# Optimization experiments

Measured on AMD Instinct MI355X. Metric: run time of the kernel, lower is better.

Reference implementation:

```python
import jax, jax.numpy as jnp
import numpy as np

N_NODES = 200_000
N_EDGES = 6_400_000
N_GRAPHS = 512


def _sage_conv(x, edge_index, Wl, bl, Wr):
    """PyG SAGEConv (mean aggr): lin_l(mean_j x_j) + lin_r(x_i).
    lin_l has bias, lin_r does not. Messages flow src -> dst."""
    src, dst = edge_index[0], edge_index[1]
    n = x.shape[0]
    # gather neighbor features [E, F] and segment-mean into dst nodes
    msg_sum = jax.ops.segment_sum(x[src], dst, num_segments=n)
    deg = jax.ops.segment_sum(jnp.ones((src.shape[0],), x.dtype), dst, num_segments=n)
    mean = msg_sum / jnp.maximum(deg, 1.0)[:, None]  # zero in-degree -> 0
    return mean @ Wl.T + bl + x @ Wr.T


def setup_inputs() -> dict:
    key = jax.random.key(0)
    ks = jax.random.split(key, 9)
    x = jax.random.normal(ks[0], (N_NODES, 1), dtype=jnp.float32)
    edge_index = jax.random.randint(ks[1], (2, N_EDGES), 0, N_NODES, dtype=jnp.int64)
    batch = jnp.sort(jax.random.randint(ks[2], (N_NODES,), 0, N_GRAPHS, dtype=jnp.int64))
    W1l = jax.random.normal(ks[3], (16, 1), dtype=jnp.float32)
    b1 = jax.random.normal(ks[4], (16,), dtype=jnp.float32)
    W1r = jax.random.normal(ks[5], (16, 1), dtype=jnp.float32)
    W2l = jax.random.normal(ks[6], (1, 16), dtype=jnp.float32)
    b2 = jax.random.normal(ks[7], (1,), dtype=jnp.float32)
    W2r = jax.random.normal(ks[8], (1, 16), dtype=jnp.float32)
    return {"x": x, "edge_index": edge_index, "batch": batch, "batch_size": N_GRAPHS,
            "W1l": W1l, "b1": b1, "W1r": W1r, "W2l": W2l, "b2": b2, "W2r": W2r}


def reference(x, edge_index, batch, batch_size, W1l, b1, W1r, W2l, b2, W2r):
    h = _sage_conv(x, edge_index, W1l, b1, W1r)          # [N, 16]
    h = jax.nn.relu(h)
    h = _sage_conv(h, edge_index, W2l, b2, W2r)          # [N, 1]
    # global_add_pool: segment-sum node features by graph id
    out = jax.ops.segment_sum(h, batch, num_segments=batch_size)  # [B, 1]
    return out
```

## Files before the change

kernel.cpp:

```cpp
#include <hip/hip_runtime.h>


#define PP        16
#define BLK       1024
#define SCAP      1024u
#define SMASK     1023u
#define TILE      (BLK * 4)
#define CBIN      16
#define CNT_ONE   (1u << 25)
#define FX_BIAS   131072
#define SCALE     4096.0f
#define INV_SCALE (1.0f / 4096.0f)

__global__ __launch_bounds__(BLK) void partition_kernel(
    const int* __restrict__ ei, const float* __restrict__ x,
    unsigned* __restrict__ xq1, unsigned* __restrict__ pairs,
    unsigned* __restrict__ tails, int E, int N, int bins, unsigned Mdiv,
    int cap) {
    extern __shared__ unsigned buf[];
    __shared__ unsigned cnt[PP], base[PP], fq[PP], gb[PP];
    const int tid = threadIdx.x;
    if (tid < PP) { cnt[tid] = 0; base[tid] = 0; }

    for (int n = blockIdx.x * BLK + tid; n < N; n += gridDim.x * BLK)
        xq1[n] = CNT_ONE + (unsigned)((int)rintf(x[n] * SCALE) + FX_BIAS);
    __syncthreads();

    int b0 = blockIdx.x * TILE;
    int e0 = b0 + tid * 4;
    int nv = E - e0; nv = nv < 0 ? 0 : (nv > 4 ? 4 : nv);
    int srcv[4], dstv[4];
    if (nv == 4 && ((E & 3) == 0)) {
        int4 s = *(const int4*)(ei + e0);
        int4 d = *(const int4*)(ei + E + e0);
        srcv[0] = s.x; srcv[1] = s.y; srcv[2] = s.z; srcv[3] = s.w;
        dstv[0] = d.x; dstv[1] = d.y; dstv[2] = d.z; dstv[3] = d.w;
    } else {
        for (int j = 0; j < nv; ++j) { srcv[j] = ei[e0 + j]; dstv[j] = ei[E + e0 + j]; }
    }
    unsigned w[4]; int part[4]; bool pend[4];
    for (int j = 0; j < 4; ++j) {
        pend[j] = (j < nv);
        if (pend[j]) {
            unsigned dst = (unsigned)dstv[j];
            unsigned pt = (unsigned)(((unsigned long long)dst * Mdiv) >> 32);
            int ld = (int)dst - (int)pt * bins;
            while (ld >= bins) { ld -= bins; ++pt; }
            while (ld < 0)     { ld += bins; --pt; }
            part[j] = (int)pt;
            w[j] = ((unsigned)srcv[j] << 14) | (unsigned)ld;
        }
    }
    for (int j = 0; j < 4; ++j) {
        if (pend[j]) {
            unsigned slot = atomicAdd(&cnt[part[j]], 1u);
            if (slot - base[part[j]] < SCAP) {
                buf[part[j] * SCAP + (slot & SMASK)] = w[j]; pend[j] = false;
            } else atomicSub(&cnt[part[j]], 1u);
        }
    }
    int npend = __syncthreads_count((int)(pend[0] | pend[1] | pend[2] | pend[3]));
    while (npend > 0) {
        if (tid < PP) {
            unsigned avail = cnt[tid] - base[tid];
            unsigned f = avail & ~511u;
            fq[tid] = f;
            if (f) gb[tid] = atomicAdd(&tails[tid], f);
        }
        __syncthreads();
        {
            int wv = tid >> 6, lane = tid & 63;
            unsigned f = fq[wv];
            if (f) {
                unsigned g0 = gb[wv], bs = base[wv];
                unsigned mx = (g0 + f <= (unsigned)cap) ? f : ((unsigned)cap > g0 ? (unsigned)cap - g0 : 0u);
                unsigned* dp = pairs + (size_t)wv * cap + g0;
                for (unsigned jj = lane; jj < mx; jj += 64)
                    dp[jj] = buf[wv * SCAP + ((bs + jj) & SMASK)];
            }
        }
        __syncthreads();
        if (tid < PP) base[tid] += fq[tid];
        __syncthreads();
        for (int j = 0; j < 4; ++j) {
            if (pend[j]) {
                unsigned slot = atomicAdd(&cnt[part[j]], 1u);
                if (slot - base[part[j]] < SCAP) {
                    buf[part[j] * SCAP + (slot & SMASK)] = w[j]; pend[j] = false;
                } else atomicSub(&cnt[part[j]], 1u);
            }
        }
        npend = __syncthreads_count((int)(pend[0] | pend[1] | pend[2] | pend[3]));
    }
    if (tid < PP) {
        unsigned avail = cnt[tid] - base[tid];
        fq[tid] = avail;
        if (avail) gb[tid] = atomicAdd(&tails[tid], avail);
    }
    __syncthreads();
    {
        int wv = tid >> 6, lane = tid & 63;
        unsigned f = fq[wv];
        if (f) {
            unsigned g0 = gb[wv], bs = base[wv];
            unsigned mx = (g0 + f <= (unsigned)cap) ? f : ((unsigned)cap > g0 ? (unsigned)cap - g0 : 0u);
            unsigned* dp = pairs + (size_t)wv * cap + g0;
            for (unsigned jj = lane; jj < mx; jj += 64)
                dp[jj] = buf[wv * SCAP + ((bs + jj) & SMASK)];
        }
    }
}

__global__ __launch_bounds__(BLK) void bin1_kernel(
    const unsigned* __restrict__ pairs, const unsigned* __restrict__ tails,
    const unsigned* __restrict__ xq1, unsigned* __restrict__ slab,
    int N, int bins, int cap) {
    extern __shared__ unsigned sb[];
    int p = blockIdx.x & (PP - 1);
    int c = blockIdx.x / PP;
    int len = (int)tails[p]; if (len > cap) len = cap;
    int st = (int)((long long)len * c / CBIN);
    int en = (int)((long long)len * (c + 1) / CBIN);
    for (int j = threadIdx.x; j < bins; j += BLK) sb[j] = 0;
    __syncthreads();
    const unsigned* bp = pairs + (size_t)p * cap;
    int st4 = (st + 3) & ~3;
    int en4 = en & ~3;
    int preEnd = st4 < en ? st4 : en;
    for (int e = st + (int)threadIdx.x; e < preEnd; e += BLK) {
        unsigned wv = bp[e];
        atomicAdd(&sb[wv & 16383u], xq1[wv >> 14]);
    }
    if (st4 < en4) {
        const uint4* bp4 = (const uint4*)(bp + st4);
        int n4 = (en4 - st4) >> 2;
        for (int e = threadIdx.x; e < n4; e += BLK) {
            uint4 wq = bp4[e];
            unsigned p0 = xq1[wq.x >> 14];
            unsigned p1 = xq1[wq.y >> 14];
            unsigned p2 = xq1[wq.z >> 14];
            unsigned p3 = xq1[wq.w >> 14];
            atomicAdd(&sb[wq.x & 16383u], p0);
            atomicAdd(&sb[wq.y & 16383u], p1);
            atomicAdd(&sb[wq.z & 16383u], p2);
            atomicAdd(&sb[wq.w & 16383u], p3);
        }
    }
    int tailSt = st4 > en4 ? st4 : en4;
    for (int e = tailSt + (int)threadIdx.x; e < en; e += BLK) {
        unsigned wv = bp[e];
        atomicAdd(&sb[wv & 16383u], xq1[wv >> 14]);
    }
    __syncthreads();
    unsigned* dst = slab + (size_t)c * N + (size_t)p * bins;
    int nb = N - p * bins; if (nb > bins) nb = bins;
    for (int j = threadIdx.x; j < nb; j += BLK) dst[j] = sb[j];
}

__global__ __launch_bounds__(BLK) void bin2_kernel(
    const unsigned* __restrict__ pairs, const unsigned* __restrict__ tails,
    const int* __restrict__ pvq, int* __restrict__ slab,
    int N, int bins, int cap) {
    extern __shared__ int sbi[];
    int p = blockIdx.x & (PP - 1);
    int c = blockIdx.x / PP;
    int len = (int)tails[p]; if (len > cap) len = cap;
    int st = (int)((long long)len * c / CBIN);
    int en = (int)((long long)len * (c + 1) / CBIN);
    for (int j = threadIdx.x; j < bins; j += BLK) sbi[j] = 0;
    __syncthreads();
    const unsigned* bp = pairs + (size_t)p * cap;
    int st4 = (st + 3) & ~3;
    int en4 = en & ~3;
    int preEnd = st4 < en ? st4 : en;
    for (int e = st + (int)threadIdx.x; e < preEnd; e += BLK) {
        unsigned wv = bp[e];
        atomicAdd(&sbi[wv & 16383u], pvq[wv >> 14]);
    }
    if (st4 < en4) {
        const uint4* bp4 = (const uint4*)(bp + st4);
        int n4 = (en4 - st4) >> 2;
        for (int e = threadIdx.x; e < n4; e += BLK) {
            uint4 wq = bp4[e];
            int p0 = pvq[wq.x >> 14];
            int p1 = pvq[wq.y >> 14];
            int p2 = pvq[wq.z >> 14];
            int p3 = pvq[wq.w >> 14];
            atomicAdd(&sbi[wq.x & 16383u], p0);
            atomicAdd(&sbi[wq.y & 16383u], p1);
            atomicAdd(&sbi[wq.z & 16383u], p2);
            atomicAdd(&sbi[wq.w & 16383u], p3);
        }
    }
    int tailSt = st4 > en4 ? st4 : en4;
    for (int e = tailSt + (int)threadIdx.x; e < en; e += BLK) {
        unsigned wv = bp[e];
        atomicAdd(&sbi[wv & 16383u], pvq[wv >> 14]);
    }
    __syncthreads();
    int* dst = slab + (size_t)c * N + (size_t)p * bins;
    int nb = N - p * bins; if (nb > bins) nb = bins;
    for (int j = threadIdx.x; j < nb; j += BLK) dst[j] = sbi[j];
}

__global__ void node_pass1_kernel(const float* __restrict__ x,
                                  const unsigned* __restrict__ slab,
                                  const float* __restrict__ W1l,
                                  const float* __restrict__ b1,
                                  const float* __restrict__ W1r,
                                  const float* __restrict__ W2l,
                                  const float* __restrict__ W2r,
                                  float* __restrict__ deg_out,
                                  int* __restrict__ pvq,
                                  float* __restrict__ qv,
                                  int N) {
    __shared__ float s_w1l[16], s_b1[16], s_w1r[16], s_w2l[16], s_w2r[16];
    if (threadIdx.x < 16) {
        s_w1l[threadIdx.x] = W1l[threadIdx.x];
        s_b1[threadIdx.x]  = b1[threadIdx.x];
        s_w1r[threadIdx.x] = W1r[threadIdx.x];
        s_w2l[threadIdx.x] = W2l[threadIdx.x];
        s_w2r[threadIdx.x] = W2r[threadIdx.x];
    }
    __syncthreads();
    int n = blockIdx.x * blockDim.x + threadIdx.x;
    if (n >= N) return;

    unsigned cnt = 0, fx = 0;
#pragma unroll
    for (int c = 0; c < CBIN; ++c) {
        unsigned w = slab[(size_t)c * N + n];
        cnt += w >> 25;
        fx  += w & (CNT_ONE - 1);
    }
    float dg  = (float)cnt;
    float sum = (float)(int)(fx - cnt * (unsigned)FX_BIAS) * INV_SCALE;
    float m   = sum / fmaxf(dg, 1.0f);

    float xv = x[n];
    float pa = 0.0f, qa = 0.0f;
#pragma unroll
    for (int f = 0; f < 16; ++f) {
        float h = fmaf(m, s_w1l[f], fmaf(xv, s_w1r[f], s_b1[f]));
        h = fmaxf(h, 0.0f);
        pa = fmaf(h, s_w2l[f], pa);
        qa = fmaf(h, s_w2r[f], qa);
    }
    deg_out[n] = dg;
    pvq[n] = (int)rintf(pa * SCALE);
    qv[n] = qa;
}

__global__ void node_pass2_kernel(const int* __restrict__ slab2,
                                  const float* __restrict__ deg,
                                  const float* __restrict__ qv,
                                  const float* __restrict__ b2,
                                  const int* __restrict__ batch,
                                  float* __restrict__ out,
                                  int N) {
    int i = blockIdx.x * blockDim.x + threadIdx.x;
    float b2v = b2[0];
    float val = 0.0f;
    int g;
    if (i < N) {
        int sacc = 0;
#pragma unroll
        for (int c = 0; c < CBIN; ++c) sacc += slab2[(size_t)c * N + i];
        float s2 = (float)sacc * INV_SCALE;
        val = s2 / fmaxf(deg[i], 1.0f) + b2v + qv[i];
        g = batch[i];
    } else {
        g = batch[N - 1];
    }
    int g0 = __shfl(g, 0);
    unsigned long long same = __ballot(g == g0);
    if (same == ~0ULL) {
        for (int off = 32; off > 0; off >>= 1) val += __shfl_down(val, off);
        if ((threadIdx.x & 63) == 0) atomicAdd(&out[g0], val);
    } else {
        atomicAdd(&out[g], val);
    }
}

extern "C" void kernel_launch(void* const* d_in, const int* in_sizes, int n_in,
                              void* d_out, int out_size, void* d_ws, size_t ws_size,
                              hipStream_t stream) {
    const float* x     = (const float*)d_in[0];
    const int*   ei    = (const int*)d_in[1];
    const int*   batch = (const int*)d_in[2];
    const float* W1l = (const float*)d_in[4];
    const float* b1  = (const float*)d_in[5];
    const float* W1r = (const float*)d_in[6];
    const float* W2l = (const float*)d_in[7];
    const float* b2  = (const float*)d_in[8];
    const float* W2r = (const float*)d_in[9];

    const int N = in_sizes[0];
    const int E = in_sizes[1] / 2;
    float* out = (float*)d_out;

    const int bins = (N + PP - 1) / PP;
    const unsigned Mdiv =
        (unsigned)(((1ULL << 32) + (unsigned)bins - 1) / (unsigned)bins);
    const int EperP = E / PP;
    int cap = ((EperP + EperP / 32 + 4096) + 1023) & ~1023;

    unsigned* pairs = (unsigned*)d_ws;
    unsigned* slab1 = pairs + (size_t)PP * cap;
    int*      slab2 = (int*)slab1;
    float* deg = (float*)(slab1 + (size_t)CBIN * N);
    int*   pvq = (int*)(deg + N);
    float* qv  = (float*)(pvq + N);
    unsigned* tails = (unsigned*)(qv + N);
    unsigned* xq1   = tails + PP;

    hipMemsetAsync(d_out, 0, (size_t)out_size * sizeof(float), stream);
    hipMemsetAsync(tails, 0, PP * sizeof(unsigned), stream);

    const int partShmem = PP * (int)SCAP * 4;
    const int binShmem  = bins * 4;
    hipFuncSetAttribute((const void*)partition_kernel,
                        hipFuncAttributeMaxDynamicSharedMemorySize, partShmem);
    hipFuncSetAttribute((const void*)bin1_kernel,
                        hipFuncAttributeMaxDynamicSharedMemorySize, binShmem);
    hipFuncSetAttribute((const void*)bin2_kernel,
                        hipFuncAttributeMaxDynamicSharedMemorySize, binShmem);

    int partBlocks = (E + TILE - 1) / TILE;
    const int NB = 256;
    int node_blocks = (N + NB - 1) / NB;

    partition_kernel<<<partBlocks, BLK, partShmem, stream>>>(ei, x, xq1, pairs,
                                                             tails, E, N, bins,
                                                             Mdiv, cap);
    bin1_kernel<<<PP * CBIN, BLK, binShmem, stream>>>(pairs, tails, xq1, slab1,
                                                      N, bins, cap);
    node_pass1_kernel<<<node_blocks, NB, 0, stream>>>(x, slab1, W1l, b1, W1r,
                                                      W2l, W2r, deg, pvq, qv, N);
    bin2_kernel<<<PP * CBIN, BLK, binShmem, stream>>>(pairs, tails, pvq, slab2,
                                                      N, bins, cap);
    node_pass2_kernel<<<node_blocks, NB, 0, stream>>>(slab2, deg, qv, b2, batch,
                                                      out, N);
}
```

Baseline: 219.8 us.

## Partition edges into 2D dst-by-src cells so bin kernels gather from LDS

Edges are now partitioned into 500 cells, split by destination partition (20) and by source block of 8192 nodes (25). Each bin block stages its source slice of features in shared memory, so the random gather of xq1/pvq reads LDS instead of global memory. The partition kernel becomes persistent with 512 blocks and uses a 32-entry ring per cell, which means more frequent flushes and a larger per-cell loop. In exchange, node passes sum 25 slabs instead of 16, cell capacity depends on a uniform-distribution estimate, and each cell flushes in small chunks.

```diff
diff --git a/kernel.cpp b/kernel.cpp
--- a/kernel.cpp
+++ b/kernel.cpp
@@ -1,12 +1,14 @@
 #include <hip/hip_runtime.h>
 
 
-#define PP        16
 #define BLK       1024
-#define SCAP      1024u
-#define SMASK     1023u
 #define TILE      (BLK * 4)
-#define CBIN      16
+#define NSB       25
+#define SBSH      13
+#define WMSK      8191u
+#define RING      32u
+#define RMSK      31u
+#define MAXC      512
 #define CNT_ONE   (1u << 25)
 #define FX_BIAS   131072
 #define SCALE     4096.0f
@@ -16,191 +18,180 @@
     const int* __restrict__ ei, const float* __restrict__ x,
     unsigned* __restrict__ xq1, unsigned* __restrict__ pairs,
     unsigned* __restrict__ tails, int E, int N, int bins, unsigned Mdiv,
-    int cap) {
+    int capC, int nc) {
     extern __shared__ unsigned buf[];
-    __shared__ unsigned cnt[PP], base[PP], fq[PP], gb[PP];
+    __shared__ unsigned cnt[MAXC], base[MAXC], fq[MAXC], gb[MAXC];
     const int tid = threadIdx.x;
-    if (tid < PP) { cnt[tid] = 0; base[tid] = 0; }
+    for (int j = tid; j < nc; j += BLK) { cnt[j] = 0; base[j] = 0; }
 
     for (int n = blockIdx.x * BLK + tid; n < N; n += gridDim.x * BLK)
         xq1[n] = CNT_ONE + (unsigned)((int)rintf(x[n] * SCALE) + FX_BIAS);
     __syncthreads();
 
-    int b0 = blockIdx.x * TILE;
-    int e0 = b0 + tid * 4;
-    int nv = E - e0; nv = nv < 0 ? 0 : (nv > 4 ? 4 : nv);
-    int srcv[4], dstv[4];
-    if (nv == 4 && ((E & 3) == 0)) {
-        int4 s = *(const int4*)(ei + e0);
-        int4 d = *(const int4*)(ei + E + e0);
-        srcv[0] = s.x; srcv[1] = s.y; srcv[2] = s.z; srcv[3] = s.w;
-        dstv[0] = d.x; dstv[1] = d.y; dstv[2] = d.z; dstv[3] = d.w;
-    } else {
-        for (int j = 0; j < nv; ++j) { srcv[j] = ei[e0 + j]; dstv[j] = ei[E + e0 + j]; }
-    }
-    unsigned w[4]; int part[4]; bool pend[4];
-    for (int j = 0; j < 4; ++j) {
-        pend[j] = (j < nv);
-        if (pend[j]) {
-            unsigned dst = (unsigned)dstv[j];
-            unsigned pt = (unsigned)(((unsigned long long)dst * Mdiv) >> 32);
-            int ld = (int)dst - (int)pt * bins;
-            while (ld >= bins) { ld -= bins; ++pt; }
-            while (ld < 0)     { ld += bins; --pt; }
-            part[j] = (int)pt;
-            w[j] = ((unsigned)srcv[j] << 14) | (unsigned)ld;
-        }
-    }
-    for (int j = 0; j < 4; ++j) {
-        if (pend[j]) {
-            unsigned slot = atomicAdd(&cnt[part[j]], 1u);
-            if (slot - base[part[j]] < SCAP) {
-                buf[part[j] * SCAP + (slot & SMASK)] = w[j]; pend[j] = false;
-            } else atomicSub(&cnt[part[j]], 1u);
-        }
-    }
-    int npend = __syncthreads_count((int)(pend[0] | pend[1] | pend[2] | pend[3]));
-    while (npend > 0) {
-        if (tid < PP) {
-            unsigned avail = cnt[tid] - base[tid];
-            unsigned f = avail & ~511u;
-            fq[tid] = f;
-            if (f) gb[tid] = atomicAdd(&tails[tid], f);
-        }
-        __syncthreads();
-        {
-            int wv = tid >> 6, lane = tid & 63;
-            unsigned f = fq[wv];
-            if (f) {
-                unsigned g0 = gb[wv], bs = base[wv];
-                unsigned mx = (g0 + f <= (unsigned)cap) ? f : ((unsigned)cap > g0 ? (unsigned)cap - g0 : 0u);
-                unsigned* dp = pairs + (size_t)wv * cap + g0;
-                for (unsigned jj = lane; jj < mx; jj += 64)
-                    dp[jj] = buf[wv * SCAP + ((bs + jj) & SMASK)];
-            }
-        }
-        __syncthreads();
-        if (tid < PP) base[tid] += fq[tid];
-        __syncthreads();
+    const int ntiles = (E + TILE - 1) / TILE;
+    for (int t = blockIdx.x; t < ntiles; t += gridDim.x) {
+        int e0 = t * TILE + tid * 4;
+        int nv = E - e0; nv = nv < 0 ? 0 : (nv > 4 ? 4 : nv);
+        int srcv[4], dstv[4];
+        if (nv == 4 && ((E & 3) == 0)) {
+            int4 s = *(const int4*)(ei + e0);
+            int4 d = *(const int4*)(ei + E + e0);
+            srcv[0] = s.x; srcv[1] = s.y; srcv[2] = s.z; srcv[3] = s.w;
+            dstv[0] = d.x; dstv[1] = d.y; dstv[2] = d.z; dstv[3] = d.w;
+        } else {
+            for (int j = 0; j < nv; ++j) { srcv[j] = ei[e0 + j]; dstv[j] = ei[E + e0 + j]; }
+        }
+        unsigned w[4]; int cell[4]; bool pend[4];
+        for (int j = 0; j < 4; ++j) {
+            pend[j] = (j < nv);
+            if (pend[j]) {
+                unsigned dst = (unsigned)dstv[j];
+                unsigned src = (unsigned)srcv[j];
+                unsigned pt = (unsigned)(((unsigned long long)dst * Mdiv) >> 32);
+                int ld = (int)dst - (int)pt * bins;
+                while (ld >= bins) { ld -= bins; ++pt; }
+                while (ld < 0)     { ld += bins; --pt; }
+                cell[j] = (int)(pt * NSB + (src >> SBSH));
+                w[j] = ((src & WMSK) << 14) | (unsigned)ld;
+            }
+        }
         for (int j = 0; j < 4; ++j) {
             if (pend[j]) {
-                unsigned slot = atomicAdd(&cnt[part[j]], 1u);
-                if (slot - base[part[j]] < SCAP) {
-                    buf[part[j] * SCAP + (slot & SMASK)] = w[j]; pend[j] = false;
-                } else atomicSub(&cnt[part[j]], 1u);
-            }
-        }
-        npend = __syncthreads_count((int)(pend[0] | pend[1] | pend[2] | pend[3]));
-    }
-    if (tid < PP) {
-        unsigned avail = cnt[tid] - base[tid];
-        fq[tid] = avail;
-        if (avail) gb[tid] = atomicAdd(&tails[tid], avail);
+                unsigned slot = atomicAdd(&cnt[cell[j]], 1u);
+                if (slot - base[cell[j]] < RING) {
+                    buf[cell[j] * RING + (slot & RMSK)] = w[j]; pend[j] = false;
+                } else atomicSub(&cnt[cell[j]], 1u);
+            }
+        }
+        int npend = __syncthreads_count((int)(pend[0] | pend[1] | pend[2] | pend[3]));
+        while (npend > 0) {
+            for (int j = tid; j < nc; j += BLK) {
+                unsigned avail = cnt[j] - base[j];
+                unsigned f = avail & ~RMSK;
+                fq[j] = f;
+                if (f) gb[j] = atomicAdd(&tails[j], f);
+            }
+            __syncthreads();
+            {
+                int wv = tid >> 6, lane = tid & 63;
+                for (int r = wv; r < nc; r += 16) {
+                    unsigned f = fq[r];
+                    if (f) {
+                        unsigned g0 = gb[r], bs = base[r];
+                        unsigned mx = (g0 + f <= (unsigned)capC) ? f : ((unsigned)capC > g0 ? (unsigned)capC - g0 : 0u);
+                        unsigned* dp = pairs + (size_t)r * capC + g0;
+                        for (unsigned jj = lane; jj < mx; jj += 64)
+                            dp[jj] = buf[r * RING + ((bs + jj) & RMSK)];
+                    }
+                }
+            }
+            __syncthreads();
+            for (int j = tid; j < nc; j += BLK) base[j] += fq[j];
+            __syncthreads();
+            for (int j = 0; j < 4; ++j) {
+                if (pend[j]) {
+                    unsigned slot = atomicAdd(&cnt[cell[j]], 1u);
+                    if (slot - base[cell[j]] < RING) {
+                        buf[cell[j] * RING + (slot & RMSK)] = w[j]; pend[j] = false;
+                    } else atomicSub(&cnt[cell[j]], 1u);
+                }
+            }
+            npend = __syncthreads_count((int)(pend[0] | pend[1] | pend[2] | pend[3]));
+        }
+    }
+    for (int j = tid; j < nc; j += BLK) {
+        unsigned avail = cnt[j] - base[j];
+        fq[j] = avail;
+        if (avail) gb[j] = atomicAdd(&tails[j], avail);
     }
     __syncthreads();
     {
         int wv = tid >> 6, lane = tid & 63;
-        unsigned f = fq[wv];
-        if (f) {
-            unsigned g0 = gb[wv], bs = base[wv];
-            unsigned mx = (g0 + f <= (unsigned)cap) ? f : ((unsigned)cap > g0 ? (unsigned)cap - g0 : 0u);
-            unsigned* dp = pairs + (size_t)wv * cap + g0;
-            for (unsigned jj = lane; jj < mx; jj += 64)
-                dp[jj] = buf[wv * SCAP + ((bs + jj) & SMASK)];
-        }
-    }
-}
-
-__global__ __launch_bounds__(BLK) void bin1_kernel(
+        for (int r = wv; r < nc; r += 16) {
+            unsigned f = fq[r];
+            if (f) {
+                unsigned g0 = gb[r], bs = base[r];
+                unsigned mx = (g0 + f <= (unsigned)capC) ? f : ((unsigned)capC > g0 ? (unsigned)capC - g0 : 0u);
+                unsigned* dp = pairs + (size_t)r * capC + g0;
+                for (unsigned jj = lane; jj < mx; jj += 64)
+                    dp[jj] = buf[r * RING + ((bs + jj) & RMSK)];
+            }
+        }
+    }
+}
+
+__global__ __launch_bounds__(BLK, 8) void bin1_kernel(
     const unsigned* __restrict__ pairs, const unsigned* __restrict__ tails,
     const unsigned* __restrict__ xq1, unsigned* __restrict__ slab,
-    int N, int bins, int cap) {
-    extern __shared__ unsigned sb[];
-    int p = blockIdx.x & (PP - 1);
-    int c = blockIdx.x / PP;
-    int len = (int)tails[p]; if (len > cap) len = cap;
-    int st = (int)((long long)len * c / CBIN);
-    int en = (int)((long long)len * (c + 1) / CBIN);
-    for (int j = threadIdx.x; j < bins; j += BLK) sb[j] = 0;
-    __syncthreads();
-    const unsigned* bp = pairs + (size_t)p * cap;
-    int st4 = (st + 3) & ~3;
-    int en4 = en & ~3;
-    int preEnd = st4 < en ? st4 : en;
-    for (int e = st + (int)threadIdx.x; e < preEnd; e += BLK) {
+    int N, int bins, int capC) {
+    extern __shared__ unsigned sm[];
+    unsigned* xs = sm;
+    unsigned* sb = sm + 8192;
+    const int tid = threadIdx.x;
+    const int cell = blockIdx.x;
+    const int p = cell / NSB;
+    const int sbk = cell - p * NSB;
+    const int wb = sbk << SBSH;
+    int nn = N - wb; if (nn > 8192) nn = 8192;
+    for (int j = tid; j < nn; j += BLK) xs[j] = xq1[wb + j];
+    for (int j = tid; j < bins; j += BLK) sb[j] = 0;
+    __syncthreads();
+    int len = (int)tails[cell]; if (len > capC) len = capC;
+    const unsigned* bp = pairs + (size_t)cell * capC;
+    int len4 = len & ~3;
+    const uint4* bp4 = (const uint4*)bp;
+    for (int e = tid; e < (len4 >> 2); e += BLK) {
+        uint4 wq = bp4[e];
+        atomicAdd(&sb[wq.x & 16383u], xs[wq.x >> 14]);
+        atomicAdd(&sb[wq.y & 16383u], xs[wq.y >> 14]);
+        atomicAdd(&sb[wq.z & 16383u], xs[wq.z >> 14]);
+        atomicAdd(&sb[wq.w & 16383u], xs[wq.w >> 14]);
+    }
+    for (int e = len4 + tid; e < len; e += BLK) {
         unsigned wv = bp[e];
-        atomicAdd(&sb[wv & 16383u], xq1[wv >> 14]);
-    }
-    if (st4 < en4) {
-        const uint4* bp4 = (const uint4*)(bp + st4);
-        int n4 = (en4 - st4) >> 2;
-        for (int e = threadIdx.x; e < n4; e += BLK) {
-            uint4 wq = bp4[e];
-            unsigned p0 = xq1[wq.x >> 14];
-            unsigned p1 = xq1[wq.y >> 14];
-            unsigned p2 = xq1[wq.z >> 14];
-            unsigned p3 = xq1[wq.w >> 14];
-            atomicAdd(&sb[wq.x & 16383u], p0);
-            atomicAdd(&sb[wq.y & 16383u], p1);
-            atomicAdd(&sb[wq.z & 16383u], p2);
-            atomicAdd(&sb[wq.w & 16383u], p3);
-        }
-    }
-    int tailSt = st4 > en4 ? st4 : en4;
-    for (int e = tailSt + (int)threadIdx.x; e < en; e += BLK) {
-        unsigned wv = bp[e];
-        atomicAdd(&sb[wv & 16383u], xq1[wv >> 14]);
-    }
-    __syncthreads();
-    unsigned* dst = slab + (size_t)c * N + (size_t)p * bins;
+        atomicAdd(&sb[wv & 16383u], xs[wv >> 14]);
+    }
+    __syncthreads();
+    unsigned* dst = slab + (size_t)sbk * N + (size_t)p * bins;
     int nb = N - p * bins; if (nb > bins) nb = bins;
-    for (int j = threadIdx.x; j < nb; j += BLK) dst[j] = sb[j];
-}
-
-__global__ __launch_bounds__(BLK) void bin2_kernel(
+    for (int j = tid; j < nb; j += BLK) dst[j] = sb[j];
+}
+
+__global__ __launch_bounds__(BLK, 8) void bin2_kernel(
     const unsigned* __restrict__ pairs, const unsigned* __restrict__ tails,
     const int* __restrict__ pvq, int* __restrict__ slab,
-    int N, int bins, int cap) {
-    extern __shared__ int sbi[];
-    int p = blockIdx.x & (PP - 1);
-    int c = blockIdx.x / PP;
-    int len = (int)tails[p]; if (len > cap) len = cap;
-    int st = (int)((long long)len * c / CBIN);
-    int en = (int)((long long)len * (c + 1) / CBIN);
-    for (int j = threadIdx.x; j < bins; j += BLK) sbi[j] = 0;
-    __syncthreads();
-    const unsigned* bp = pairs + (size_t)p * cap;
-    int st4 = (st + 3) & ~3;
-    int en4 = en & ~3;
-    int preEnd = st4 < en ? st4 : en;
-    for (int e = st + (int)threadIdx.x; e < preEnd; e += BLK) {
+    int N, int bins, int capC) {
+    extern __shared__ unsigned sm[];
+    int* ps = (int*)sm;
+    int* sbi = (int*)(sm + 8192);
+    const int tid = threadIdx.x;
+    const int cell = blockIdx.x;
+    const int p = cell / NSB;
+    const int sbk = cell - p * NSB;
+    const int wb = sbk << SBSH;
+    int nn = N - wb; if (nn > 8192) nn = 8192;
+    for (int j = tid; j < nn; j += BLK) ps[j] = pvq[wb + j];
+    for (int j = tid; j < bins; j += BLK) sbi[j] = 0;
+    __syncthreads();
+    int len = (int)tails[cell]; if (len > capC) len = capC;
+    const unsigned* bp = pairs + (size_t)cell * capC;
+    int len4 = len & ~3;
+    const uint4* bp4 = (const uint4*)bp;
+    for (int e = tid; e < (len4 >> 2); e += BLK) {
+        uint4 wq = bp4[e];
+        atomicAdd(&sbi[wq.x & 16383u], ps[wq.x >> 14]);
+        atomicAdd(&sbi[wq.y & 16383u], ps[wq.y >> 14]);
+        atomicAdd(&sbi[wq.z & 16383u], ps[wq.z >> 14]);
+        atomicAdd(&sbi[wq.w & 16383u], ps[wq.w >> 14]);
+    }
+    for (int e = len4 + tid; e < len; e += BLK) {
         unsigned wv = bp[e];
-        atomicAdd(&sbi[wv & 16383u], pvq[wv >> 14]);
-    }
-    if (st4 < en4) {
-        const uint4* bp4 = (const uint4*)(bp + st4);
-        int n4 = (en4 - st4) >> 2;
-        for (int e = threadIdx.x; e < n4; e += BLK) {
-            uint4 wq = bp4[e];
-            int p0 = pvq[wq.x >> 14];
-            int p1 = pvq[wq.y >> 14];
-            int p2 = pvq[wq.z >> 14];
-            int p3 = pvq[wq.w >> 14];
-            atomicAdd(&sbi[wq.x & 16383u], p0);
-            atomicAdd(&sbi[wq.y & 16383u], p1);
-            atomicAdd(&sbi[wq.z & 16383u], p2);
-            atomicAdd(&sbi[wq.w & 16383u], p3);
-        }
-    }
-    int tailSt = st4 > en4 ? st4 : en4;
-    for (int e = tailSt + (int)threadIdx.x; e < en; e += BLK) {
-        unsigned wv = bp[e];
-        atomicAdd(&sbi[wv & 16383u], pvq[wv >> 14]);
-    }
-    __syncthreads();
-    int* dst = slab + (size_t)c * N + (size_t)p * bins;
+        atomicAdd(&sbi[wv & 16383u], ps[wv >> 14]);
+    }
+    __syncthreads();
+    int* dst = slab + (size_t)sbk * N + (size_t)p * bins;
     int nb = N - p * bins; if (nb > bins) nb = bins;
-    for (int j = threadIdx.x; j < nb; j += BLK) dst[j] = sbi[j];
+    for (int j = tid; j < nb; j += BLK) dst[j] = sbi[j];
 }
 
 __global__ void node_pass1_kernel(const float* __restrict__ x,
@@ -228,7 +219,7 @@
 
     unsigned cnt = 0, fx = 0;
 #pragma unroll
-    for (int c = 0; c < CBIN; ++c) {
+    for (int c = 0; c < NSB; ++c) {
         unsigned w = slab[(size_t)c * N + n];
         cnt += w >> 25;
         fx  += w & (CNT_ONE - 1);
@@ -265,7 +256,7 @@
     if (i < N) {
         int sacc = 0;
 #pragma unroll
-        for (int c = 0; c < CBIN; ++c) sacc += slab2[(size_t)c * N + i];
+        for (int c = 0; c < NSB; ++c) sacc += slab2[(size_t)c * N + i];
         float s2 = (float)sacc * INV_SCALE;
         val = s2 / fmaxf(deg[i], 1.0f) + b2v + qv[i];
         g = batch[i];
@@ -299,26 +290,28 @@
     const int E = in_sizes[1] / 2;
     float* out = (float*)d_out;
 
-    const int bins = (N + PP - 1) / PP;
+    const int pp   = 20;
+    const int bins = (N + pp - 1) / pp;
+    const int nc   = pp * NSB;
     const unsigned Mdiv =
         (unsigned)(((1ULL << 32) + (unsigned)bins - 1) / (unsigned)bins);
-    const int EperP = E / PP;
-    int cap = ((EperP + EperP / 32 + 4096) + 1023) & ~1023;
+    long long cellExp = ((long long)E / pp) * 8192 / N;
+    int capC = (int)((cellExp + 2048 + 1023) & ~1023LL);
 
     unsigned* pairs = (unsigned*)d_ws;
-    unsigned* slab1 = pairs + (size_t)PP * cap;
+    unsigned* slab1 = pairs + (size_t)nc * capC;
     int*      slab2 = (int*)slab1;
-    float* deg = (float*)(slab1 + (size_t)CBIN * N);
+    float* deg = (float*)(slab1 + (size_t)NSB * N);
     int*   pvq = (int*)(deg + N);
     float* qv  = (float*)(pvq + N);
-    unsigned* tails = (unsigned*)(qv + N);
-    unsigned* xq1   = tails + PP;
+    unsigned* xq1   = (unsigned*)(qv + N);
+    unsigned* tails = xq1 + N;
 
     hipMemsetAsync(d_out, 0, (size_t)out_size * sizeof(float), stream);
-    hipMemsetAsync(tails, 0, PP * sizeof(unsigned), stream);
-
-    const int partShmem = PP * (int)SCAP * 4;
-    const int binShmem  = bins * 4;
+    hipMemsetAsync(tails, 0, nc * sizeof(unsigned), stream);
+
+    const int partShmem = nc * (int)RING * 4;
+    const int binShmem  = (8192 + bins) * 4;
     hipFuncSetAttribute((const void*)partition_kernel,
                         hipFuncAttributeMaxDynamicSharedMemorySize, partShmem);
     hipFuncSetAttribute((const void*)bin1_kernel,
@@ -326,19 +319,19 @@
     hipFuncSetAttribute((const void*)bin2_kernel,
                         hipFuncAttributeMaxDynamicSharedMemorySize, binShmem);
 
-    int partBlocks = (E + TILE - 1) / TILE;
+    const int partBlocks = 512;
     const int NB = 256;
     int node_blocks = (N + NB - 1) / NB;
 
     partition_kernel<<<partBlocks, BLK, partShmem, stream>>>(ei, x, xq1, pairs,
                                                              tails, E, N, bins,
-                                                             Mdiv, cap);
-    bin1_kernel<<<PP * CBIN, BLK, binShmem, stream>>>(pairs, tails, xq1, slab1,
-                                                      N, bins, cap);
+                                                             Mdiv, capC, nc);
+    bin1_kernel<<<nc, BLK, binShmem, stream>>>(pairs, tails, xq1, slab1,
+                                               N, bins, capC);
     node_pass1_kernel<<<node_blocks, NB, 0, stream>>>(x, slab1, W1l, b1, W1r,
                                                       W2l, W2r, deg, pvq, qv, N);
-    bin2_kernel<<<PP * CBIN, BLK, binShmem, stream>>>(pairs, tails, pvq, slab2,
-                                                      N, bins, cap);
+    bin2_kernel<<<nc, BLK, binShmem, stream>>>(pairs, tails, pvq, slab2,
+                                               N, bins, capC);
     node_pass2_kernel<<<node_blocks, NB, 0, stream>>>(slab2, deg, qv, b2, batch,
                                                       out, N);
 }
```

Result: faster. 214.1 us (-2.6%).
